# Kernel tuning notes

Hardware: AMD Instinct MI355X
Metric: run time of the kernel (lower is better)

## Reference

```python
import jax, jax.numpy as jnp
import numpy as np
from jax import lax

N = 50000        # num nodes
E = 800000       # edges per relation (no self loops; N self loops appended)
R = 3            # num_relations
F_IN = 256       # feature_size
C = 128          # hid_dim / channels
B = 4096         # batch_nodes
DT = 0.25
NSTEPS = 4       # n = ceil(time/dt) = ceil(1.0/0.25)


def setup_inputs() -> dict:
    key = jax.random.key(0)
    k1, k2, k3, k4, k5, k6, k7, k8 = jax.random.split(key, 8)
    features = jax.random.normal(k1, (N, F_IN), dtype=jnp.float32)
    # edges with no self loops: dst = (src + off) mod N, off in [1, N)
    src = jax.random.randint(k2, (R, E), 0, N)
    off = jax.random.randint(k3, (R, E), 1, N)
    dst = (src + off) % N
    edge_index = jnp.stack([src, dst], axis=1).astype(jnp.int64)  # [R, 2, E]
    batch_nodes = jax.random.randint(k4, (B,), 0, N).astype(jnp.int64)
    s = 1.0 / np.sqrt(F_IN)
    lin0_w = jax.random.normal(k5, (R, C, F_IN), dtype=jnp.float32) * s
    lin0_b = jax.random.normal(k6, (R, C), dtype=jnp.float32) * 0.01
    lin1_w = jax.random.normal(k7, (R, C, F_IN), dtype=jnp.float32) * s
    lin1_b = jax.random.normal(k8, (R, C), dtype=jnp.float32) * 0.01
    return {"features": features, "edge_index": edge_index, "batch_nodes": batch_nodes,
            "lin0_w": lin0_w, "lin0_b": lin0_b, "lin1_w": lin1_w, "lin1_b": lin1_b}


def _propagate(x, row, col, w):
    # out[i] = sum_{e: col[e]==i} w[e] * x[row[e]]   (gather-scale-scatter SpMM)
    return jax.ops.segment_sum(w[:, None] * x[row], col, num_segments=N)


def _wave_pde(x, row, col, w0, b0, w1, b1):
    # add_remaining_self_loops(fill=0.0): self loops appended at end with weight 0
    loops = jnp.arange(N, dtype=row.dtype)
    row_f = jnp.concatenate([row, loops])
    col_f = jnp.concatenate([col, loops])
    w_f = jnp.concatenate([jnp.ones((E,), x.dtype), jnp.zeros((N,), x.dtype)])
    # sym normalization: D^-1/2 A D^-1/2 (deg over col)
    deg = jax.ops.segment_sum(w_f, col_f, num_segments=N)
    dinv = jnp.where(deg > 0, lax.rsqrt(jnp.maximum(deg, 1e-30)), 0.0)
    w_norm = dinv[row_f] * w_f * dinv[col_f]
    # set_init_value
    phi0 = x @ w0.T + b0
    phi1 = x @ w1.T + b1
    # exp_conv_0 (exp_init=True): w' = dt^2*w/2; diag += 1; x1 = dt*phi1 + prop(phi0)
    w_init = (DT * DT * 0.5) * w_norm
    w_init = w_init.at[E:].add(1.0)
    x1 = DT * phi1 + _propagate(phi0, row_f, col_f, w_init)
    # time-stepping convs: w'' = dt^2*w; diag += 2; x_next = prop(x) - x_pre
    w_step = (DT * DT) * w_norm
    w_step = w_step.at[E:].add(2.0)

    def step(carry, _):
        xc, xp = carry
        xn = _propagate(xc, row_f, col_f, w_step) - xp
        return (xn, xc), None

    (x_out, _), _ = lax.scan(step, (x1, phi0), None, length=NSTEPS - 1)
    return x_out


def reference(features, edge_index, batch_nodes, lin0_w, lin0_b, lin1_w, lin1_b):
    # eval mode: dropout is identity
    embeds = []
    for r in range(R):
        row = edge_index[r, 0]
        col = edge_index[r, 1]
        x = _wave_pde(features, row, col, lin0_w[r], lin0_b[r], lin1_w[r], lin1_b[r])
        embeds.append(x[batch_nodes])  # [B, C]
    multi = jnp.stack(embeds, axis=1)  # [B, R, C]
    return multi.reshape(B, R * C)
```

## Files before the change

kernel.cpp:

```cpp
#include <hip/hip_runtime.h>
#include <hip/hip_bf16.h>

#define N_NODES 50000
#define N_EDGES 800000
#define N_REL   3
#define F_IN    256
#define CH      128
#define BATCH   4096
#define DT      0.25f

typedef __bf16 bf16x8 __attribute__((ext_vector_type(8)));
typedef float f32x4 __attribute__((ext_vector_type(4)));

__device__ __forceinline__ ushort f2bf(float f) {
  unsigned u = __float_as_uint(f);
  return (ushort)((u + 0x7FFFu + ((u >> 16) & 1u)) >> 16);
}
__device__ __forceinline__ float bf2f(ushort h) {
  return __uint_as_float((unsigned)h << 16);
}

__global__ void k_detect(const int* __restrict__ ei, int* __restrict__ flag) {
  int lane = threadIdx.x;
  int v = ei[2 * lane + 1];
  unsigned long long m = __ballot(v != 0);
  if (lane == 0) flag[0] = (m == 0ull) ? 1 : 0;
}

__global__ void k_hist3(const int* __restrict__ ei, const int* __restrict__ flag,
                        int* __restrict__ deg3) {
  int e = blockIdx.x * 256 + threadIdx.x;
  int r = blockIdx.y;
  if (e >= N_EDGES) return;
  long ci = (long)r * 2 * N_EDGES + N_EDGES + e;
  int d = flag[0] ? ei[2 * ci] : ei[ci];
  atomicAdd(&deg3[r * N_NODES + d], 1);
}

__global__ void k_dinv3(const int* __restrict__ deg3, float* __restrict__ dinv3,
                        int* __restrict__ flag) {
  int i = blockIdx.x * blockDim.x + threadIdx.x;
  if (i >= 3 * N_NODES) return;
  int d = deg3[i];
  if (d > 0) {
    dinv3[i] = rsqrtf((float)d);
  } else {
    dinv3[i] = 0.0f;
    atomicOr(&flag[1], 1);
  }
}

__global__ void k_scan3(const int* __restrict__ deg3, int* __restrict__ off3) {
  __shared__ int sm[1024];
  const int* deg = deg3 + blockIdx.x * N_NODES;
  int* off = off3 + blockIdx.x * (N_NODES + 1);
  int tid = threadIdx.x;
  const int PER = (N_NODES + 1023) / 1024;
  int base = tid * PER;
  int s = 0;
  for (int i = 0; i < PER; ++i) { int idx = base + i; if (idx < N_NODES) s += deg[idx]; }
  sm[tid] = s;
  __syncthreads();
  for (int d = 1; d < 1024; d <<= 1) {
    int v = 0;
    if (tid >= d) v = sm[tid - d];
    __syncthreads();
    sm[tid] += v;
    __syncthreads();
  }
  int run = sm[tid] - s;
  for (int i = 0; i < PER; ++i) {
    int idx = base + i;
    if (idx < N_NODES) { off[idx] = run; run += deg[idx]; }
  }
  if (tid == 1023) off[N_NODES] = run;
}

__global__ void k_fill3(const int* __restrict__ ei, const int* __restrict__ flag,
                        const int* __restrict__ off3, int* __restrict__ cur3,
                        const float* __restrict__ dinv3, void* __restrict__ csrv) {
  int e = blockIdx.x * 256 + threadIdx.x;
  int r = blockIdx.y;
  if (e >= N_EDGES) return;
  int i64 = flag[0], iso = flag[1];
  long ri = (long)r * 2 * N_EDGES + e;
  long ci = ri + N_EDGES;
  int s = i64 ? ei[2 * ri] : ei[ri];
  int d = i64 ? ei[2 * ci] : ei[ci];
  int pos = atomicAdd(&cur3[r * N_NODES + d], 1);
  int slot = off3[r * (N_NODES + 1) + d] + pos;
  if (iso) {
    const float* dinv = dinv3 + r * N_NODES;
    ((int2*)csrv)[(size_t)r * N_EDGES + slot] =
        make_int2(s, __float_as_int(dinv[s] * dinv[d]));
  } else {
    ((int*)csrv)[(size_t)r * N_EDGES + slot] = s;
  }
}

__global__ __launch_bounds__(256) void k_phi_mfma(
    const float* __restrict__ X, const float* __restrict__ W0,
    const float* __restrict__ b0, const float* __restrict__ W1,
    const float* __restrict__ b1, const float* __restrict__ dinv,
    const int* __restrict__ flag, float* __restrict__ P0,
    float* __restrict__ P1) {
  __shared__ ushort Ah[128 * 32], Al[128 * 32], Bh[128 * 32], Bl[128 * 32];
  const int tid = threadIdx.x;
  const int m0 = blockIdx.x * 128;
  const float* W = blockIdx.y ? W1 : W0;
  const float* bias = blockIdx.y ? b1 : b0;
  float* P = blockIdx.y ? P1 : P0;
  const int wid = tid >> 6, lane = tid & 63;
  const int wr = wid >> 1, wc = wid & 1;
  const int lr = lane & 15, k8 = lane >> 4;
  const int rt = tid >> 1, kb = (tid & 1) * 16;
  const bool mok = (m0 + rt) < N_NODES;
  const float* Xrow = X + (size_t)(m0 + rt) * F_IN;
  const float* Wrow = W + (size_t)rt * F_IN;
  f32x4 acc[4][4] = {};
  for (int k0 = 0; k0 < F_IN; k0 += 32) {
    float4 xa[4], wb[4];
#pragma unroll
    for (int j = 0; j < 4; ++j) {
      xa[j] = mok ? *(const float4*)(Xrow + k0 + kb + 4 * j)
                  : make_float4(0.f, 0.f, 0.f, 0.f);
      wb[j] = *(const float4*)(Wrow + k0 + kb + 4 * j);
    }
    if (k0) __syncthreads();
#pragma unroll
    for (int j = 0; j < 4; ++j) {
      int idx = rt * 32 + kb + 4 * j;
      ushort h0 = f2bf(xa[j].x), h1 = f2bf(xa[j].y), h2 = f2bf(xa[j].z), h3 = f2bf(xa[j].w);
      *(ushort4*)&Ah[idx] = make_ushort4(h0, h1, h2, h3);
      *(ushort4*)&Al[idx] =
          make_ushort4(f2bf(xa[j].x - bf2f(h0)), f2bf(xa[j].y - bf2f(h1)),
                       f2bf(xa[j].z - bf2f(h2)), f2bf(xa[j].w - bf2f(h3)));
      ushort g0 = f2bf(wb[j].x), g1 = f2bf(wb[j].y), g2 = f2bf(wb[j].z), g3 = f2bf(wb[j].w);
      *(ushort4*)&Bh[idx] = make_ushort4(g0, g1, g2, g3);
      *(ushort4*)&Bl[idx] =
          make_ushort4(f2bf(wb[j].x - bf2f(g0)), f2bf(wb[j].y - bf2f(g1)),
                       f2bf(wb[j].z - bf2f(g2)), f2bf(wb[j].w - bf2f(g3)));
    }
    __syncthreads();
    bf16x8 ah[4], al[4], bh[4], bl[4];
#pragma unroll
    for (int i = 0; i < 4; ++i) {
      int ao = (wr * 64 + i * 16 + lr) * 32 + k8 * 8;
      int bo = (wc * 64 + i * 16 + lr) * 32 + k8 * 8;
      ah[i] = *(const bf16x8*)&Ah[ao];
      al[i] = *(const bf16x8*)&Al[ao];
      bh[i] = *(const bf16x8*)&Bh[bo];
      bl[i] = *(const bf16x8*)&Bl[bo];
    }
#pragma unroll
    for (int i = 0; i < 4; ++i)
#pragma unroll
      for (int j = 0; j < 4; ++j) {
        acc[i][j] = __builtin_amdgcn_mfma_f32_16x16x32_bf16(ah[i], bh[j], acc[i][j], 0, 0, 0);
        acc[i][j] = __builtin_amdgcn_mfma_f32_16x16x32_bf16(ah[i], bl[j], acc[i][j], 0, 0, 0);
        acc[i][j] = __builtin_amdgcn_mfma_f32_16x16x32_bf16(al[i], bh[j], acc[i][j], 0, 0, 0);
      }
  }
  int iso = flag[1];
  float rsc[4][4];
#pragma unroll
  for (int i = 0; i < 4; ++i)
#pragma unroll
    for (int q = 0; q < 4; ++q) {
      int m = m0 + wr * 64 + i * 16 + k8 * 4 + q;
      rsc[i][q] = (m < N_NODES && !iso) ? dinv[m] : 1.0f;
    }
#pragma unroll
  for (int j = 0; j < 4; ++j) {
    int ch = wc * 64 + j * 16 + lr;
    float bv = bias[ch];
#pragma unroll
    for (int i = 0; i < 4; ++i) {
      int mbase = m0 + wr * 64 + i * 16 + k8 * 4;
#pragma unroll
      for (int q = 0; q < 4; ++q) {
        int m = mbase + q;
        if (m < N_NODES) P[(size_t)m * CH + ch] = (acc[i][j][q] + bv) * rsc[i][q];
      }
    }
  }
}

__device__ __forceinline__ void prop_accum(
    const float* __restrict__ xc, const void* __restrict__ csrv, int r, int iso,
    int e0, int e1, int g, int l, float4& acc0, float4& acc1) {
  if (!iso) {
    const int* csr = (const int*)csrv + (size_t)r * N_EDGES;
    for (int e = e0; e < e1; e += 16) {
      int lim = e1 - 1;
      int src[4]; float wgt[4];
#pragma unroll
      for (int u = 0; u < 4; ++u) {
        int ee = e + 4 * u + g;
        src[u] = csr[min(ee, lim)];
        wgt[u] = (ee <= lim) ? 1.f : 0.f;
      }
      float4 va[4], vb[4];
#pragma unroll
      for (int u = 0; u < 4; ++u) {
        const float4* rs = (const float4*)(xc + (size_t)src[u] * CH);
        va[u] = rs[l];
        vb[u] = rs[l + 16];
      }
#pragma unroll
      for (int u = 0; u < 4; ++u) {
        float w0 = wgt[u];
        acc0.x = fmaf(w0, va[u].x, acc0.x); acc0.y = fmaf(w0, va[u].y, acc0.y);
        acc0.z = fmaf(w0, va[u].z, acc0.z); acc0.w = fmaf(w0, va[u].w, acc0.w);
        acc1.x = fmaf(w0, vb[u].x, acc1.x); acc1.y = fmaf(w0, vb[u].y, acc1.y);
        acc1.z = fmaf(w0, vb[u].z, acc1.z); acc1.w = fmaf(w0, vb[u].w, acc1.w);
      }
    }
  } else {
    const int2* csr = (const int2*)csrv + (size_t)r * N_EDGES;
    for (int e = e0; e < e1; e += 16) {
      int lim = e1 - 1;
      int2 pm[4]; float wgt[4];
#pragma unroll
      for (int u = 0; u < 4; ++u) {
        int ee = e + 4 * u + g;
        pm[u] = csr[min(ee, lim)];
        wgt[u] = (ee <= lim) ? __int_as_float(pm[u].y) : 0.f;
      }
      float4 va[4], vb[4];
#pragma unroll
      for (int u = 0; u < 4; ++u) {
        const float4* rs = (const float4*)(xc + (size_t)pm[u].x * CH);
        va[u] = rs[l];
        vb[u] = rs[l + 16];
      }
#pragma unroll
      for (int u = 0; u < 4; ++u) {
        float w0 = wgt[u];
        acc0.x = fmaf(w0, va[u].x, acc0.x); acc0.y = fmaf(w0, va[u].y, acc0.y);
        acc0.z = fmaf(w0, va[u].z, acc0.z); acc0.w = fmaf(w0, va[u].w, acc0.w);
        acc1.x = fmaf(w0, vb[u].x, acc1.x); acc1.y = fmaf(w0, vb[u].y, acc1.y);
        acc1.z = fmaf(w0, vb[u].z, acc1.z); acc1.w = fmaf(w0, vb[u].w, acc1.w);
      }
    }
  }
}

__global__ __launch_bounds__(256, 6) void k_prop(
    const float* __restrict__ xc, const float* __restrict__ other,
    float* __restrict__ out, const int* __restrict__ off,
    const void* __restrict__ csrv, const int* __restrict__ flag, int r,
    float wscale, float aself, float beta) {
  int node = blockIdx.x * 4 + (threadIdx.x >> 6);
  if (node >= N_NODES) return;
  int iso = flag[1];
  int lane = threadIdx.x & 63;
  int g = lane >> 4, l = lane & 15;
  int e0 = off[node], e1 = off[node + 1];
  size_t base = (size_t)node * CH;
  int go = (g & 1) * 64;
  float4 sv = *(const float4*)(xc + base + go + 4 * l);
  float4 ov = *(const float4*)(other + base + go + 4 * l);
  float4 acc0 = make_float4(0.f, 0.f, 0.f, 0.f);
  float4 acc1 = make_float4(0.f, 0.f, 0.f, 0.f);
  prop_accum(xc, csrv, r, iso, e0, e1, g, l, acc0, acc1);
#pragma unroll
  for (int m = 16; m < 64; m <<= 1) {
    acc0.x += __shfl_xor(acc0.x, m); acc0.y += __shfl_xor(acc0.y, m);
    acc0.z += __shfl_xor(acc0.z, m); acc0.w += __shfl_xor(acc0.w, m);
    acc1.x += __shfl_xor(acc1.x, m); acc1.y += __shfl_xor(acc1.y, m);
    acc1.z += __shfl_xor(acc1.z, m); acc1.w += __shfl_xor(acc1.w, m);
  }
  float ws2 = iso ? wscale : ((e1 > e0) ? wscale / (float)(e1 - e0) : 0.f);
  if (g == 0) {
    float4 o;
    o.x = ws2 * acc0.x + aself * sv.x + beta * ov.x;
    o.y = ws2 * acc0.y + aself * sv.y + beta * ov.y;
    o.z = ws2 * acc0.z + aself * sv.z + beta * ov.z;
    o.w = ws2 * acc0.w + aself * sv.w + beta * ov.w;
    *(float4*)(out + base + 4 * l) = o;
  } else if (g == 1) {
    float4 o;
    o.x = ws2 * acc1.x + aself * sv.x + beta * ov.x;
    o.y = ws2 * acc1.y + aself * sv.y + beta * ov.y;
    o.z = ws2 * acc1.z + aself * sv.z + beta * ov.z;
    o.w = ws2 * acc1.w + aself * sv.w + beta * ov.w;
    *(float4*)(out + base + 64 + 4 * l) = o;
  }
}

__global__ __launch_bounds__(256) void k_gprop(
    const float* __restrict__ y3, const float* __restrict__ y2,
    const int* __restrict__ off, const void* __restrict__ csrv,
    const int* __restrict__ flag, const int* __restrict__ batch,
    float* __restrict__ out, int r, float wscale, float aself, float beta) {
  int b = blockIdx.x * 4 + (threadIdx.x >> 6);
  if (b >= BATCH) return;
  int i64 = flag[0], iso = flag[1];
  int node = i64 ? batch[2 * b] : batch[b];
  int lane = threadIdx.x & 63;
  int g = lane >> 4, l = lane & 15;
  int e0 = off[node], e1 = off[node + 1];
  size_t base = (size_t)node * CH;
  int go = (g & 1) * 64;
  float4 sv = *(const float4*)(y3 + base + go + 4 * l);
  float4 ov = *(const float4*)(y2 + base + go + 4 * l);
  float4 acc0 = make_float4(0.f, 0.f, 0.f, 0.f);
  float4 acc1 = make_float4(0.f, 0.f, 0.f, 0.f);
  prop_accum(y3, csrv, r, iso, e0, e1, g, l, acc0, acc1);
#pragma unroll
  for (int m = 16; m < 64; m <<= 1) {
    acc0.x += __shfl_xor(acc0.x, m); acc0.y += __shfl_xor(acc0.y, m);
    acc0.z += __shfl_xor(acc0.z, m); acc0.w += __shfl_xor(acc0.w, m);
    acc1.x += __shfl_xor(acc1.x, m); acc1.y += __shfl_xor(acc1.y, m);
    acc1.z += __shfl_xor(acc1.z, m); acc1.w += __shfl_xor(acc1.w, m);
  }
  int deg = e1 - e0;
  float ws2 = iso ? wscale : ((deg > 0) ? wscale / (float)deg : 0.f);
  float osc = iso ? 1.0f : sqrtf((float)deg);
  float* orow = out + (size_t)b * (N_REL * CH) + r * CH;
  if (g == 0) {
    float4 o;
    o.x = osc * (ws2 * acc0.x + aself * sv.x + beta * ov.x);
    o.y = osc * (ws2 * acc0.y + aself * sv.y + beta * ov.y);
    o.z = osc * (ws2 * acc0.z + aself * sv.z + beta * ov.z);
    o.w = osc * (ws2 * acc0.w + aself * sv.w + beta * ov.w);
    *(float4*)(orow + 4 * l) = o;
  } else if (g == 1) {
    float4 o;
    o.x = osc * (ws2 * acc1.x + aself * sv.x + beta * ov.x);
    o.y = osc * (ws2 * acc1.y + aself * sv.y + beta * ov.y);
    o.z = osc * (ws2 * acc1.z + aself * sv.z + beta * ov.z);
    o.w = osc * (ws2 * acc1.w + aself * sv.w + beta * ov.w);
    *(float4*)(orow + 64 + 4 * l) = o;
  }
}

extern "C" void kernel_launch(void* const* d_in, const int* in_sizes, int n_in,
                              void* d_out, int out_size, void* d_ws, size_t ws_size,
                              hipStream_t stream) {
  const float* features   = (const float*)d_in[0];
  const int*   edge_index = (const int*)d_in[1];
  const int*   batch_nodes= (const int*)d_in[2];
  const float* lin0_w     = (const float*)d_in[3];
  const float* lin0_b     = (const float*)d_in[4];
  const float* lin1_w     = (const float*)d_in[5];
  const float* lin1_b     = (const float*)d_in[6];
  float* out = (float*)d_out;

  char* w = (char*)d_ws;
  size_t o = 0;
  auto nxt = [&](size_t bytes) {
    char* p = w + o;
    o = (o + bytes + 255) & ~(size_t)255;
    return p;
  };
  int*   flag  = (int*)  nxt(256);
  int*   deg3  = (int*)  nxt((size_t)3 * N_NODES * 4);
  int*   cur3  = (int*)  nxt((size_t)3 * N_NODES * 4);
  float* dinv3 = (float*)nxt((size_t)3 * N_NODES * 4);
  int*   off3  = (int*)  nxt((size_t)3 * (N_NODES + 1) * 4);
  void*  csr   = (void*) nxt((size_t)3 * N_EDGES * 8);
  float* P0    = (float*)nxt((size_t)N_NODES * CH * 4);
  float* P1    = (float*)nxt((size_t)N_NODES * CH * 4);
  float* Ab    = (float*)nxt((size_t)N_NODES * CH * 4);

  hipMemsetAsync(flag, 0, 8, stream);
  hipMemsetAsync(deg3, 0, (size_t)3 * N_NODES * 4, stream);
  hipMemsetAsync(cur3, 0, (size_t)3 * N_NODES * 4, stream);
  k_detect<<<1, 64, 0, stream>>>(edge_index, flag);
  k_hist3<<<dim3((N_EDGES + 255) / 256, 3), 256, 0, stream>>>(edge_index, flag, deg3);
  k_dinv3<<<(3 * N_NODES + 255) / 256, 256, 0, stream>>>(deg3, dinv3, flag);
  k_scan3<<<3, 1024, 0, stream>>>(deg3, off3);
  k_fill3<<<dim3((N_EDGES + 255) / 256, 3), 256, 0, stream>>>(edge_index, flag, off3,
                                                              cur3, dinv3, csr);

  const float h2 = DT * DT;
  for (int r = 0; r < N_REL; ++r) {
    const int* offr = off3 + r * (N_NODES + 1);
    k_phi_mfma<<<dim3((N_NODES + 127) / 128, 2), 256, 0, stream>>>(
        features, lin0_w + (size_t)r * CH * F_IN, lin0_b + (size_t)r * CH,
        lin1_w + (size_t)r * CH * F_IN, lin1_b + (size_t)r * CH,
        dinv3 + r * N_NODES, flag, P0, P1);
    k_prop<<<(N_NODES + 3) / 4, 256, 0, stream>>>(P0, P1, Ab, offr, csr, flag, r,
                                                  0.5f * h2, 1.0f, DT);
    k_prop<<<(N_NODES + 3) / 4, 256, 0, stream>>>(Ab, P0, P0, offr, csr, flag, r,
                                                  h2, 2.0f, -1.0f);
    k_prop<<<(N_NODES + 3) / 4, 256, 0, stream>>>(P0, Ab, Ab, offr, csr, flag, r,
                                                  h2, 2.0f, -1.0f);
    k_gprop<<<(BATCH + 3) / 4, 256, 0, stream>>>(Ab, P0, offr, csr, flag,
                                                 batch_nodes, out, r,
                                                 h2, 2.0f, -1.0f);
  }
}
```

Baseline: 1.190 ms.

## Batch all relations into single propagation launches and range-partition CSR build

```diff
diff --git a/kernel.cpp b/kernel.cpp
--- a/kernel.cpp
+++ b/kernel.cpp
@@ -8,6 +8,8 @@
 #define CH      128
 #define BATCH   4096
 #define DT      0.25f
+#define NRANGE  8
+#define RSPAN   6250
 
 typedef __bf16 bf16x8 __attribute__((ext_vector_type(8)));
 typedef float f32x4 __attribute__((ext_vector_type(4)));
@@ -27,14 +29,16 @@
   if (lane == 0) flag[0] = (m == 0ull) ? 1 : 0;
 }
 
-__global__ void k_hist3(const int* __restrict__ ei, const int* __restrict__ flag,
-                        int* __restrict__ deg3) {
-  int e = blockIdx.x * 256 + threadIdx.x;
+__global__ void k_hist3x(const int* __restrict__ ei, const int* __restrict__ flag,
+                         int* __restrict__ deg3) {
+  int b = blockIdx.x;
+  int q = b & (NRANGE - 1), chunk = b >> 3;
+  int e = chunk * 256 + threadIdx.x;
   int r = blockIdx.y;
   if (e >= N_EDGES) return;
   long ci = (long)r * 2 * N_EDGES + N_EDGES + e;
   int d = flag[0] ? ei[2 * ci] : ei[ci];
-  atomicAdd(&deg3[r * N_NODES + d], 1);
+  if (d / RSPAN == q) atomicAdd(&deg3[r * N_NODES + d], 1);
 }
 
 __global__ void k_dinv3(const int* __restrict__ deg3, float* __restrict__ dinv3,
@@ -76,17 +80,20 @@
   if (tid == 1023) off[N_NODES] = run;
 }
 
-__global__ void k_fill3(const int* __restrict__ ei, const int* __restrict__ flag,
-                        const int* __restrict__ off3, int* __restrict__ cur3,
-                        const float* __restrict__ dinv3, void* __restrict__ csrv) {
-  int e = blockIdx.x * 256 + threadIdx.x;
+__global__ void k_fill3x(const int* __restrict__ ei, const int* __restrict__ flag,
+                         const int* __restrict__ off3, int* __restrict__ cur3,
+                         const float* __restrict__ dinv3, void* __restrict__ csrv) {
+  int b = blockIdx.x;
+  int q = b & (NRANGE - 1), chunk = b >> 3;
+  int e = chunk * 256 + threadIdx.x;
   int r = blockIdx.y;
   if (e >= N_EDGES) return;
   int i64 = flag[0], iso = flag[1];
   long ri = (long)r * 2 * N_EDGES + e;
   long ci = ri + N_EDGES;
+  int d = i64 ? ei[2 * ci] : ei[ci];
+  if (d / RSPAN != q) return;
   int s = i64 ? ei[2 * ri] : ei[ri];
-  int d = i64 ? ei[2 * ci] : ei[ci];
   int pos = atomicAdd(&cur3[r * N_NODES + d], 1);
   int slot = off3[r * (N_NODES + 1) + d] + pos;
   if (iso) {
@@ -247,12 +254,17 @@
 }
 
 __global__ __launch_bounds__(256, 6) void k_prop(
-    const float* __restrict__ xc, const float* __restrict__ other,
-    float* __restrict__ out, const int* __restrict__ off,
-    const void* __restrict__ csrv, const int* __restrict__ flag, int r,
-    float wscale, float aself, float beta) {
+    const float* __restrict__ xcb, const float* __restrict__ otherb,
+    float* __restrict__ outb, const int* __restrict__ off3,
+    const void* __restrict__ csrv, const int* __restrict__ flag, int rel0,
+    size_t slab, float wscale, float aself, float beta) {
   int node = blockIdx.x * 4 + (threadIdx.x >> 6);
   if (node >= N_NODES) return;
+  int rel = rel0 + blockIdx.y;
+  const float* xc = xcb + (size_t)blockIdx.y * slab;
+  const float* other = otherb + (size_t)blockIdx.y * slab;
+  float* out = outb + (size_t)blockIdx.y * slab;
+  const int* off = off3 + rel * (N_NODES + 1);
   int iso = flag[1];
   int lane = threadIdx.x & 63;
   int g = lane >> 4, l = lane & 15;
@@ -263,7 +275,7 @@
   float4 ov = *(const float4*)(other + base + go + 4 * l);
   float4 acc0 = make_float4(0.f, 0.f, 0.f, 0.f);
   float4 acc1 = make_float4(0.f, 0.f, 0.f, 0.f);
-  prop_accum(xc, csrv, r, iso, e0, e1, g, l, acc0, acc1);
+  prop_accum(xc, csrv, rel, iso, e0, e1, g, l, acc0, acc1);
 #pragma unroll
   for (int m = 16; m < 64; m <<= 1) {
     acc0.x += __shfl_xor(acc0.x, m); acc0.y += __shfl_xor(acc0.y, m);
@@ -290,12 +302,17 @@
 }
 
 __global__ __launch_bounds__(256) void k_gprop(
-    const float* __restrict__ y3, const float* __restrict__ y2,
-    const int* __restrict__ off, const void* __restrict__ csrv,
+    const float* __restrict__ y3b, const float* __restrict__ y2b,
+    const int* __restrict__ off3, const void* __restrict__ csrv,
     const int* __restrict__ flag, const int* __restrict__ batch,
-    float* __restrict__ out, int r, float wscale, float aself, float beta) {
+    float* __restrict__ out, int rel0, size_t slab,
+    float wscale, float aself, float beta) {
   int b = blockIdx.x * 4 + (threadIdx.x >> 6);
   if (b >= BATCH) return;
+  int rel = rel0 + blockIdx.y;
+  const float* y3 = y3b + (size_t)blockIdx.y * slab;
+  const float* y2 = y2b + (size_t)blockIdx.y * slab;
+  const int* off = off3 + rel * (N_NODES + 1);
   int i64 = flag[0], iso = flag[1];
   int node = i64 ? batch[2 * b] : batch[b];
   int lane = threadIdx.x & 63;
@@ -307,7 +324,7 @@
   float4 ov = *(const float4*)(y2 + base + go + 4 * l);
   float4 acc0 = make_float4(0.f, 0.f, 0.f, 0.f);
   float4 acc1 = make_float4(0.f, 0.f, 0.f, 0.f);
-  prop_accum(y3, csrv, r, iso, e0, e1, g, l, acc0, acc1);
+  prop_accum(y3, csrv, rel, iso, e0, e1, g, l, acc0, acc1);
 #pragma unroll
   for (int m = 16; m < 64; m <<= 1) {
     acc0.x += __shfl_xor(acc0.x, m); acc0.y += __shfl_xor(acc0.y, m);
@@ -318,7 +335,7 @@
   int deg = e1 - e0;
   float ws2 = iso ? wscale : ((deg > 0) ? wscale / (float)deg : 0.f);
   float osc = iso ? 1.0f : sqrtf((float)deg);
-  float* orow = out + (size_t)b * (N_REL * CH) + r * CH;
+  float* orow = out + (size_t)b * (N_REL * CH) + rel * CH;
   if (g == 0) {
     float4 o;
     o.x = osc * (ws2 * acc0.x + aself * sv.x + beta * ov.x);
@@ -348,6 +365,14 @@
   const float* lin1_b     = (const float*)d_in[6];
   float* out = (float*)d_out;
 
+  const size_t slabElems = (size_t)N_NODES * CH;
+  const size_t fixedBytes = 256 + 4 * (((size_t)3 * N_NODES * 4 + 255) & ~(size_t)255)
+                            + (((size_t)3 * N_EDGES * 8 + 255) & ~(size_t)255) + 4096;
+  const size_t fusedNeed = fixedBytes + 2 * 3 * slabElems * 4;
+  const bool fused = ws_size >= fusedNeed;
+  const size_t slab = fused ? slabElems : 0;
+  const int nslab = fused ? 3 : 1;
+
   char* w = (char*)d_ws;
   size_t o = 0;
   auto nxt = [&](size_t bytes) {
@@ -361,35 +386,56 @@
   float* dinv3 = (float*)nxt((size_t)3 * N_NODES * 4);
   int*   off3  = (int*)  nxt((size_t)3 * (N_NODES + 1) * 4);
   void*  csr   = (void*) nxt((size_t)3 * N_EDGES * 8);
-  float* P0    = (float*)nxt((size_t)N_NODES * CH * 4);
-  float* P1    = (float*)nxt((size_t)N_NODES * CH * 4);
-  float* Ab    = (float*)nxt((size_t)N_NODES * CH * 4);
+  float* A     = (float*)nxt((size_t)nslab * slabElems * 4);
+  float* B     = (float*)nxt((size_t)nslab * slabElems * 4);
 
   hipMemsetAsync(flag, 0, 8, stream);
   hipMemsetAsync(deg3, 0, (size_t)3 * N_NODES * 4, stream);
   hipMemsetAsync(cur3, 0, (size_t)3 * N_NODES * 4, stream);
   k_detect<<<1, 64, 0, stream>>>(edge_index, flag);
-  k_hist3<<<dim3((N_EDGES + 255) / 256, 3), 256, 0, stream>>>(edge_index, flag, deg3);
+  const int NCHUNK = (N_EDGES + 255) / 256;
+  k_hist3x<<<dim3(NCHUNK * NRANGE, 3), 256, 0, stream>>>(edge_index, flag, deg3);
   k_dinv3<<<(3 * N_NODES + 255) / 256, 256, 0, stream>>>(deg3, dinv3, flag);
   k_scan3<<<3, 1024, 0, stream>>>(deg3, off3);
-  k_fill3<<<dim3((N_EDGES + 255) / 256, 3), 256, 0, stream>>>(edge_index, flag, off3,
-                                                              cur3, dinv3, csr);
+  k_fill3x<<<dim3(NCHUNK * NRANGE, 3), 256, 0, stream>>>(edge_index, flag, off3,
+                                                         cur3, dinv3, csr);
 
   const float h2 = DT * DT;
   for (int r = 0; r < N_REL; ++r) {
-    const int* offr = off3 + r * (N_NODES + 1);
+    float* Ar = A + (size_t)(fused ? r : 0) * slabElems;
+    float* Br = B + (size_t)(fused ? r : 0) * slabElems;
+    if (!fused && r > 0) break;
     k_phi_mfma<<<dim3((N_NODES + 127) / 128, 2), 256, 0, stream>>>(
         features, lin0_w + (size_t)r * CH * F_IN, lin0_b + (size_t)r * CH,
         lin1_w + (size_t)r * CH * F_IN, lin1_b + (size_t)r * CH,
-        dinv3 + r * N_NODES, flag, P0, P1);
-    k_prop<<<(N_NODES + 3) / 4, 256, 0, stream>>>(P0, P1, Ab, offr, csr, flag, r,
-                                                  0.5f * h2, 1.0f, DT);
-    k_prop<<<(N_NODES + 3) / 4, 256, 0, stream>>>(Ab, P0, P0, offr, csr, flag, r,
-                                                  h2, 2.0f, -1.0f);
-    k_prop<<<(N_NODES + 3) / 4, 256, 0, stream>>>(P0, Ab, Ab, offr, csr, flag, r,
-                                                  h2, 2.0f, -1.0f);
-    k_gprop<<<(BATCH + 3) / 4, 256, 0, stream>>>(Ab, P0, offr, csr, flag,
-                                                 batch_nodes, out, r,
-                                                 h2, 2.0f, -1.0f);
-  }
-}
+        dinv3 + r * N_NODES, flag, Ar, Br);
+  }
+
+  if (fused) {
+    k_prop<<<dim3((N_NODES + 3) / 4, 3), 256, 0, stream>>>(
+        A, B, B, off3, csr, flag, 0, slab, 0.5f * h2, 1.0f, DT);
+    k_prop<<<dim3((N_NODES + 3) / 4, 3), 256, 0, stream>>>(
+        B, A, A, off3, csr, flag, 0, slab, h2, 2.0f, -1.0f);
+    k_prop<<<dim3((N_NODES + 3) / 4, 3), 256, 0, stream>>>(
+        A, B, B, off3, csr, flag, 0, slab, h2, 2.0f, -1.0f);
+    k_gprop<<<dim3((BATCH + 3) / 4, 3), 256, 0, stream>>>(
+        B, A, off3, csr, flag, batch_nodes, out, 0, slab, h2, 2.0f, -1.0f);
+  } else {
+    for (int r = 0; r < N_REL; ++r) {
+      if (r > 0) {
+        k_phi_mfma<<<dim3((N_NODES + 127) / 128, 2), 256, 0, stream>>>(
+            features, lin0_w + (size_t)r * CH * F_IN, lin0_b + (size_t)r * CH,
+            lin1_w + (size_t)r * CH * F_IN, lin1_b + (size_t)r * CH,
+            dinv3 + r * N_NODES, flag, A, B);
+      }
+      k_prop<<<dim3((N_NODES + 3) / 4, 1), 256, 0, stream>>>(
+          A, B, B, off3, csr, flag, r, 0, 0.5f * h2, 1.0f, DT);
+      k_prop<<<dim3((N_NODES + 3) / 4, 1), 256, 0, stream>>>(
+          B, A, A, off3, csr, flag, r, 0, h2, 2.0f, -1.0f);
+      k_prop<<<dim3((N_NODES + 3) / 4, 1), 256, 0, stream>>>(
+          A, B, B, off3, csr, flag, r, 0, h2, 2.0f, -1.0f);
+      k_gprop<<<dim3((BATCH + 3) / 4, 1), 256, 0, stream>>>(
+          B, A, off3, csr, flag, batch_nodes, out, r, 0, h2, 2.0f, -1.0f);
+    }
+  }
+}
```

Result: faster. 1.136 ms (-4.5%).
